# Performance work log

Hardware: AMD Instinct MI355X
Metric: run time of the kernel (lower is better)

The kernel has to match this reference:

```python
import jax, jax.numpy as jnp
import numpy as np

EPS = 1e-5

def instance_norm(x):
    # x: [B, n, C]; InstanceNorm1d normalizes over the n (length) axis per channel, no affine
    mean = jnp.mean(x, axis=1, keepdims=True)
    var = jnp.var(x, axis=1, keepdims=True)  # biased variance, matches torch
    return (x - mean) / jnp.sqrt(var + EPS)

def gat_layer(h, w, a_src, a_dst, b):
    # h: [B, n, d_in]; w: [H, d_in, d_out]; a_src/a_dst: [H, d_out, 1]; b: [d_out]
    h_ = jnp.einsum('bnd,hdk->bhnk', h, w)               # [B, H, n, d_out]
    s_src = jnp.einsum('bhnk,hk->bhn', h_, a_src[..., 0])  # [B, H, n]
    s_dst = jnp.einsum('bhnk,hk->bhn', h_, a_dst[..., 0])  # [B, H, n]
    attn = s_src[:, :, :, None] + s_dst[:, :, None, :]    # [B, H, n, n]
    attn = jax.nn.leaky_relu(attn, negative_slope=0.2)
    attn = jax.nn.softmax(attn, axis=-1)
    return jnp.einsum('bhnm,bhmk->bhnk', attn, h_) + b    # [B, H, n, d_out]

def setup_inputs() -> dict:
    key = jax.random.key(0)
    ks = jax.random.split(key, 7)
    B, N = 4, 4096
    x = jax.random.normal(ks[0], (B, N, 64), dtype=jnp.float32)
    g = 1.414
    def xavier(k, shape):
        fan_in, fan_out = shape[-2], shape[-1]
        lim = g * np.sqrt(6.0 / (fan_in + fan_out))
        return jax.random.uniform(k, shape, jnp.float32, -lim, lim)
    return {
        'x': x,
        'w0': xavier(ks[1], (4, 64, 32)),
        'a_src0': xavier(ks[2], (4, 32, 1)),
        'a_dst0': xavier(ks[3], (4, 32, 1)),
        'b0': jnp.zeros((32,), jnp.float32),
        'w1': xavier(ks[4], (1, 128, 64)),
        'a_src1': xavier(ks[5], (1, 64, 1)),
        'a_dst1': xavier(ks[6], (1, 64, 1)),
        'b1': jnp.zeros((64,), jnp.float32),
    }

def reference(x, w0, a_src0, a_dst0, b0, w1, a_src1, a_dst1, b1):
    B, N = x.shape[:2]
    # layer 0: norm -> GAT(4 heads) -> concat heads -> ELU
    h = instance_norm(x)
    h = gat_layer(h, w0, a_src0, a_dst0, b0)              # [B, 4, N, 32]
    h = jnp.transpose(h, (0, 2, 1, 3)).reshape(B, N, -1)  # [B, N, 128]
    h = jax.nn.elu(h)
    # layer 1: norm -> GAT(1 head) -> squeeze head
    h = instance_norm(h)
    h = gat_layer(h, w1, a_src1, a_dst1, b1)              # [B, 1, N, 64]
    return h[:, 0]                                        # [B, N, 64]
```

## Files before the change

kernel.cpp:

```cpp
#include <hip/hip_runtime.h>
#include <math.h>

#define N_ 4096

static constexpr size_t OFF_HP0    = 2048;
static constexpr size_t OFF_ELU    = 2048;
static constexpr size_t OFF_SS0    = 2099200;
static constexpr size_t OFF_SD0    = 2164736;
static constexpr size_t OFF_RUNS0  = 2230272;
static constexpr size_t OFF_SV0    = 2361344;
static constexpr size_t OFF_PM0    = 2426880;
static constexpr size_t OFF_EP0    = 2492416;
static constexpr size_t OFF_EN0    = 2557952;
static constexpr size_t OFF_CPP0   = 2623488;
static constexpr size_t OFF_CPN0   = 2689040;
static constexpr size_t OFF_RAWP0  = 2754592;
static constexpr size_t OFF_RAWN0  = 2885664;
static constexpr size_t OFF_BP0    = 3016736;
static constexpr size_t OFF_BN0    = 3148320;
static constexpr size_t OFF_TPP0   = 3279904;
static constexpr size_t OFF_TPN0   = 5377568;
static constexpr size_t OFF_HP1    = 3279904;
static constexpr size_t OFF_SS1    = 4328480;
static constexpr size_t OFF_SD1    = 4344864;
static constexpr size_t OFF_RUNS1  = 4361248;
static constexpr size_t OFF_SV1    = 4394016;
static constexpr size_t OFF_PM1    = 4410400;
static constexpr size_t OFF_EP1    = 4426784;
static constexpr size_t OFF_EN1    = 4443168;
static constexpr size_t OFF_CPP1   = 4459552;
static constexpr size_t OFF_CPN1   = 4475940;
static constexpr size_t OFF_RAWP1  = 4492328;
static constexpr size_t OFF_RAWN1  = 4557864;
static constexpr size_t OFF_BP1    = 4623400;
static constexpr size_t OFF_BN1    = 4689192;
static constexpr size_t OFF_TPP1   = 4754984;
static constexpr size_t OFF_TPN1   = 5803816;
static constexpr size_t OFF_S0P    = 6852648;
static constexpr size_t OFF_S1P    = 6869032;

__device__ __forceinline__ unsigned f2s(float f){
  unsigned u=__float_as_uint(f);
  return u^((u&0x80000000u)?0xFFFFFFFFu:0x80000000u);
}
__device__ __forceinline__ float s2f(unsigned s){
  unsigned u=(s&0x80000000u)?(s^0x80000000u):~s;
  return __uint_as_float(u);
}

template<int C>
__global__ void kstats(const float* __restrict__ x, float* __restrict__ statsP){
  int blk=blockIdx.x; int b=blk>>5;
  int tid=threadIdx.x;
  const int RPT=256/C;
  const int IT=128/RPT;
  int c=tid%C, rl=tid/C;
  const float* xb=x+(size_t)b*N_*C;
  float s1=0.f,s2=0.f;
  int r0=(blk&31)*128+rl;
  for(int i=0;i<IT;i++){
    float v=xb[(size_t)(r0+i*RPT)*C+c];
    s1+=v;s2+=v*v;
  }
  __shared__ float sh1[256],sh2[256];
  sh1[tid]=s1;sh2[tid]=s2;__syncthreads();
  if(tid<C){
    float a1=0.f,a2=0.f;
    for(int g=0;g<RPT;g++){a1+=sh1[g*C+tid];a2+=sh2[g*C+tid];}
    statsP[((size_t)blk*C+tid)*2+0]=a1;
    statsP[((size_t)blk*C+tid)*2+1]=a2;
  }
}

__global__ void __launch_bounds__(256) kproj0(
                       const float* __restrict__ x, const float* __restrict__ statsP,
                       const float* __restrict__ w0, const float* __restrict__ asrc,
                       const float* __restrict__ adst, float* __restrict__ hp,
                       float* __restrict__ ss, float* __restrict__ sd){
  __shared__ float4 w4[2048];
  __shared__ float4 av4[64];
  __shared__ float mean[64],rstd[64];
  __shared__ float red1[256],red2[256];
  int tid=threadIdx.x;
  const float4* wg=(const float4*)w0;
  for(int i=tid;i<2048;i+=256) w4[i]=wg[i];
  if(tid<32) av4[tid]=((const float4*)asrc)[tid];
  else if(tid<64) av4[tid]=((const float4*)adst)[tid-32];
  int gid=blockIdx.x*256+tid;
  int b=gid>>14, h=(gid>>12)&3, n=gid&4095;
  {
    int tc=tid&63, tg=tid>>6;
    float a1=0.f,a2=0.f;
    #pragma unroll 2
    for(int g=tg*8;g<tg*8+8;g++){
      a1+=statsP[((size_t)(b*32+g)*64+tc)*2+0];
      a2+=statsP[((size_t)(b*32+g)*64+tc)*2+1];
    }
    red1[tid]=a1; red2[tid]=a2;
  }
  __syncthreads();
  if(tid<64){
    float s1=red1[tid]+red1[tid+64]+red1[tid+128]+red1[tid+192];
    float s2=red2[tid]+red2[tid+64]+red2[tid+128]+red2[tid+192];
    float mu=s1*(1.0f/N_);
    float var=s2*(1.0f/N_)-mu*mu;
    mean[tid]=mu; rstd[tid]=rsqrtf(var+1e-5f);
  }
  __syncthreads();
  const float4* hr4=(const float4*)(x+((size_t)(b*N_+n))*64);
  float4 acc[8];
  #pragma unroll
  for(int q=0;q<8;q++) acc[q]=make_float4(0.f,0.f,0.f,0.f);
  #pragma unroll
  for(int ch=0;ch<4;ch++){
    float4 t[4];
    #pragma unroll
    for(int j=0;j<4;j++) t[j]=hr4[ch*4+j];
    #pragma unroll
    for(int j=0;j<4;j++){
      int d0=ch*16+j*4;
      float hv[4];
      hv[0]=(t[j].x-mean[d0+0])*rstd[d0+0];
      hv[1]=(t[j].y-mean[d0+1])*rstd[d0+1];
      hv[2]=(t[j].z-mean[d0+2])*rstd[d0+2];
      hv[3]=(t[j].w-mean[d0+3])*rstd[d0+3];
      #pragma unroll
      for(int dd=0;dd<4;dd++){
        float hvv=hv[dd];
        #pragma unroll
        for(int q=0;q<8;q++){
          float4 wv=w4[(h*64+d0+dd)*8+q];
          acc[q].x+=hvv*wv.x;acc[q].y+=hvv*wv.y;acc[q].z+=hvv*wv.z;acc[q].w+=hvv*wv.w;
        }
      }
    }
  }
  float ssv=0.f,sdv=0.f;
  #pragma unroll
  for(int q=0;q<8;q++){
    float4 a1=av4[h*8+q],a2=av4[32+h*8+q];
    ssv+=acc[q].x*a1.x+acc[q].y*a1.y+acc[q].z*a1.z+acc[q].w*a1.w;
    sdv+=acc[q].x*a2.x+acc[q].y*a2.y+acc[q].z*a2.z+acc[q].w*a2.w;
  }
  int p=b*4+h;
  float4* o4=(float4*)(hp+((size_t)p*N_+n)*32);
  #pragma unroll
  for(int q=0;q<8;q++) o4[q]=acc[q];
  ss[(size_t)p*N_+n]=ssv; sd[(size_t)p*N_+n]=sdv;
}

__global__ void __launch_bounds__(256) kproj1(
                       const float* __restrict__ x, const float* __restrict__ statsP,
                       const float* __restrict__ w1, const float* __restrict__ asrc,
                       const float* __restrict__ adst, float* __restrict__ hp,
                       float* __restrict__ ss, float* __restrict__ sd){
  __shared__ float4 w4[2048];
  __shared__ float wa[128],wd[128],mean[128],rstd[128];
  __shared__ float red1[256],red2[256];
  int tid=threadIdx.x;
  const float4* wg=(const float4*)w1;
  for(int i=tid;i<2048;i+=256) w4[i]=wg[i];
  int gid=blockIdx.x*256+tid;
  int b=gid>>14, q4=(gid>>12)&3, n=gid&4095;
  {
    int tc=tid&127, tg=tid>>7;
    float a1=0.f,a2=0.f;
    #pragma unroll 4
    for(int g=tg*16;g<tg*16+16;g++){
      a1+=statsP[((size_t)(b*32+g)*128+tc)*2+0];
      a2+=statsP[((size_t)(b*32+g)*128+tc)*2+1];
    }
    red1[tid]=a1; red2[tid]=a2;
  }
  __syncthreads();
  if(tid<128){
    float s1a=0.f,s2a=0.f;
    for(int k=0;k<64;k++){float wv=w1[tid*64+k];s1a+=wv*asrc[k];s2a+=wv*adst[k];}
    wa[tid]=s1a;wd[tid]=s2a;
    float s1=red1[tid]+red1[tid+128];
    float s2=red2[tid]+red2[tid+128];
    float mu=s1*(1.0f/N_);
    float var=s2*(1.0f/N_)-mu*mu;
    mean[tid]=mu; rstd[tid]=rsqrtf(var+1e-5f);
  }
  __syncthreads();
  const float4* hr4=(const float4*)(x+((size_t)(b*N_+n))*128);
  float4 acc[4];
  #pragma unroll
  for(int q=0;q<4;q++) acc[q]=make_float4(0.f,0.f,0.f,0.f);
  float s1=0.f,s2=0.f;
  #pragma unroll
  for(int ch=0;ch<8;ch++){
    float4 t[4];
    #pragma unroll
    for(int j=0;j<4;j++) t[j]=hr4[ch*4+j];
    #pragma unroll
    for(int j=0;j<4;j++){
      int d0=ch*16+j*4;
      float hv[4];
      hv[0]=(t[j].x-mean[d0+0])*rstd[d0+0];
      hv[1]=(t[j].y-mean[d0+1])*rstd[d0+1];
      hv[2]=(t[j].z-mean[d0+2])*rstd[d0+2];
      hv[3]=(t[j].w-mean[d0+3])*rstd[d0+3];
      #pragma unroll
      for(int dd=0;dd<4;dd++){
        float hvv=hv[dd]; int d=d0+dd;
        s1+=hvv*wa[d]; s2+=hvv*wd[d];
        #pragma unroll
        for(int q=0;q<4;q++){
          float4 wv=w4[d*16+q4*4+q];
          acc[q].x+=hvv*wv.x;acc[q].y+=hvv*wv.y;acc[q].z+=hvv*wv.z;acc[q].w+=hvv*wv.w;
        }
      }
    }
  }
  float4* o4=(float4*)(hp+((size_t)(b*N_+n))*64+q4*16);
  #pragma unroll
  for(int q=0;q<4;q++) o4[q]=acc[q];
  if(q4==0){
    ss[(size_t)b*N_+n]=s1;sd[(size_t)b*N_+n]=s2;
  }
}

__global__ void __launch_bounds__(256) ksort_runs(const float* __restrict__ sdst,
                                                  unsigned long long* __restrict__ runs){
  __shared__ unsigned long long sm[1024];
  int p=blockIdx.x>>2, run=blockIdx.x&3;
  int tid=threadIdx.x;
  const float* s=sdst+(size_t)p*N_+run*1024;
  for(int l=tid;l<1024;l+=256){
    unsigned key=f2s(s[l]);
    sm[l]=((unsigned long long)key<<32)|(unsigned)(run*1024+l);
  }
  for(unsigned k=2;k<=1024u;k<<=1)
    for(unsigned j=k>>1;j>0;j>>=1){
      __syncthreads();
      for(unsigned t=tid;t<512u;t+=256u){
        unsigned i=((t&~(j-1))<<1)|(t&(j-1));
        unsigned q=i|j;
        bool up=((i&k)==0);
        unsigned long long a=sm[i],b=sm[q];
        if((a>b)==up){sm[i]=b;sm[q]=a;}
      }
    }
  __syncthreads();
  unsigned long long* rg=runs+(size_t)p*N_+run*1024;
  for(int l=tid;l<1024;l+=256) rg[l]=sm[l];
}

__global__ void __launch_bounds__(1024) kmerge(const unsigned long long* __restrict__ runs,
    float* __restrict__ sv, unsigned* __restrict__ perm,
    float* __restrict__ eP, float* __restrict__ eN){
  __shared__ unsigned long long sm[4096];
  int p=blockIdx.x>>2, cg=blockIdx.x&3;
  int tid=threadIdx.x;
  const unsigned long long* rg=runs+(size_t)p*N_;
  for(int l=tid;l<4096;l+=1024) sm[l]=rg[l];
  __syncthreads();
  unsigned long long e=sm[cg*1024+tid];
  int rank=tid;
  #pragma unroll
  for(int o=0;o<4;o++){
    if(o==cg) continue;
    const unsigned long long* base=sm+o*1024;
    int lo=0,hi=1024;
    while(lo<hi){int mid=(lo+hi)>>1; if(base[mid]<e) lo=mid+1; else hi=mid;}
    rank+=lo;
  }
  unsigned long long mk=sm[1023];
  if(sm[2047]>mk) mk=sm[2047];
  if(sm[3071]>mk) mk=sm[3071];
  if(sm[4095]>mk) mk=sm[4095];
  float m=s2f((unsigned)(mk>>32));
  float v=s2f((unsigned)(e>>32));
  size_t o=(size_t)p*N_+rank;
  sv[o]=v;
  perm[o]=(unsigned)(e&0xffffffffu);
  eP[o]=expf(v-m);
  eN[o]=expf(0.2f*(v-m));
}

__global__ void __launch_bounds__(1024) kcounts(const float* __restrict__ eP,
    const float* __restrict__ eN, float* __restrict__ CPP, float* __restrict__ CPN){
  __shared__ float sp[1024],sn[1024];
  int p=blockIdx.x, t=threadIdx.x;
  float4 e4=((const float4*)(eP+(size_t)p*N_))[t];
  float4 n4=((const float4*)(eN+(size_t)p*N_))[t];
  float lp=e4.x+e4.y+e4.z+e4.w;
  float ln=n4.x+n4.y+n4.z+n4.w;
  sp[t]=lp; sn[t]=ln; __syncthreads();
  for(int off=1;off<1024;off<<=1){
    float vp=(t>=off)?sp[t-off]:0.f;
    float vn=(t>=off)?sn[t-off]:0.f;
    __syncthreads();
    sp[t]+=vp; sn[t]+=vn;
    __syncthreads();
  }
  float bp=sp[t]-lp, bn=sn[t]-ln;
  size_t o=(size_t)p*4097+t*4;
  float a=bp;          CPP[o+0]=a;
  a+=e4.x;             CPP[o+1]=a;
  a+=e4.y;             CPP[o+2]=a;
  a+=e4.z;             CPP[o+3]=a;
  a=bn;                CPN[o+0]=a;
  a+=n4.x;             CPN[o+1]=a;
  a+=n4.y;             CPN[o+2]=a;
  a+=n4.z;             CPN[o+3]=a;
  if(t==1023){CPP[(size_t)p*4097+4096]=sp[1023]; CPN[(size_t)p*4097+4096]=sn[1023];}
}

__global__ void __launch_bounds__(256) ktables0(const unsigned* __restrict__ perm,
    const float* __restrict__ eP, const float* __restrict__ eN,
    const float* __restrict__ hp, float* __restrict__ TPP, float* __restrict__ TPN,
    float* __restrict__ rawP, float* __restrict__ rawN){
  int gw=(blockIdx.x*256+threadIdx.x)>>6;
  int lane=threadIdx.x&63, half=lane>>5, ch=lane&31;
  int cglob=gw*2+half;
  int p=cglob>>8, c=cglob&255;
  float aP=0.f,aN=0.f;
  for(int q=0;q<16;q++){
    int r=c*16+q;
    size_t ro=(size_t)p*N_+r;
    float ep=eP[ro],en=eN[ro];
    unsigned pr=perm[ro];
    float hv=hp[((size_t)p*N_+pr)*32+ch];
    size_t to=((size_t)p*4097+r)*32+ch;
    TPP[to]=aP; TPN[to]=aN;
    aP+=ep*hv; aN+=en*hv;
  }
  size_t bo=((size_t)p*256+c)*32+ch;
  rawP[bo]=aP; rawN[bo]=aN;
}

__global__ void __launch_bounds__(256) ktables1(const unsigned* __restrict__ perm,
    const float* __restrict__ eP, const float* __restrict__ eN,
    const float* __restrict__ hp, float* __restrict__ TPP, float* __restrict__ TPN,
    float* __restrict__ rawP, float* __restrict__ rawN){
  int wid=(blockIdx.x*256+threadIdx.x)>>6;
  int lane=threadIdx.x&63;
  int p=wid>>8, c=wid&255;
  float aP=0.f,aN=0.f;
  for(int q=0;q<16;q++){
    int r=c*16+q;
    size_t ro=(size_t)p*N_+r;
    float ep=eP[ro],en=eN[ro];
    unsigned pr=perm[ro];
    float hv=hp[((size_t)p*N_+pr)*64+lane];
    size_t to=((size_t)p*4097+r)*64+lane;
    TPP[to]=aP; TPN[to]=aN;
    aP+=ep*hv; aN+=en*hv;
  }
  size_t bo=((size_t)p*256+c)*64+lane;
  rawP[bo]=aP; rawN[bo]=aN;
}

template<int D>
__global__ void __launch_bounds__(256) kscan(const float* __restrict__ rawP,
    const float* __restrict__ rawN, float* __restrict__ bP, float* __restrict__ bN,
    float* __restrict__ TPP, float* __restrict__ TPN){
  extern __shared__ float sm[];
  int p=blockIdx.x, tid=threadIdx.x;
  for(int pass=0;pass<2;pass++){
    const float* src=pass?rawN:rawP;
    float* dst=pass?bN:bP;
    float* tp=pass?TPN:TPP;
    __syncthreads();
    for(int i=tid;i<256*D;i+=256){
      sm[i]=src[(size_t)p*256*D+i];
    }
    __syncthreads();
    if(tid<D){
      float r=0.f;
      for(int c=0;c<256;c++){
        dst[((size_t)p*257+c)*D+tid]=r;
        r+=sm[c*D+tid];
      }
      dst[((size_t)p*257+256)*D+tid]=0.f;
      tp[((size_t)p*4097+4096)*D+tid]=r;
    }
  }
}

__global__ void __launch_bounds__(256) keval0(const float* __restrict__ ss,
                       const float* __restrict__ sv,
                       const float* __restrict__ bP, const float* __restrict__ bN,
                       const float* __restrict__ TPP, const float* __restrict__ TPN,
                       const float* __restrict__ CPP, const float* __restrict__ CPN,
                       const float* __restrict__ bias, float* __restrict__ out){
  int gw=(blockIdx.x*256+threadIdx.x)>>6;
  int lane=threadIdx.x&63, half=lane>>5, ch=lane&31;
  int row=gw*2+half;
  int p=row>>12, i=row&4095;
  int b=p>>2, h=p&3;
  const float* svp=sv+(size_t)p*N_;
  float ssrc=ss[(size_t)p*N_+i];
  float m=svp[4095];
  float xx=ssrc+m;
  float M=xx>0.f?xx:0.2f*xx;
  float fpos=expf(xx-M),fneg=expf(0.2f*xx-M);
  float th=-ssrc;
  float s1v=svp[ch*128+127];
  unsigned long long bal=__ballot(s1v<=th);
  int c1=half?(int)__popcll(bal>>32):(int)__popcll(bal&0xFFFFFFFFull);
  int lo;
  if(c1>=32){ lo=4096; }
  else{
    float s2v=svp[c1*128+ch*4+3];
    unsigned long long bal2=__ballot(s2v<=th);
    int c2=half?(int)__popcll(bal2>>32):(int)__popcll(bal2&0xFFFFFFFFull);
    int base=c1*128+c2*4;
    float4 qv=*((const float4*)(svp+base));
    int c3=(qv.x<=th)+(qv.y<=th)+(qv.z<=th)+(qv.w<=th);
    lo=base+c3;
  }
  int c=lo>>4;
  float relP=TPP[((size_t)p*4097+lo)*32+ch];
  float relN=TPN[((size_t)p*4097+lo)*32+ch];
  float baP=bP[((size_t)p*257+c)*32+ch];
  float baN=bN[((size_t)p*257+c)*32+ch];
  float tot=TPP[((size_t)p*4097+4096)*32+ch];
  float CPl=CPP[(size_t)p*4097+lo];
  float CNl=CPN[(size_t)p*4097+lo];
  float CT =CPP[(size_t)p*4097+4096];
  float denom=fpos*(CT-CPl)+fneg*CNl;
  float v=fpos*(tot-(baP+relP))+fneg*(baN+relN);
  float r=v/denom+bias[ch];
  r=r>0.f?r:expm1f(r);
  out[((size_t)(b*N_+i))*128+h*32+ch]=r;
}

__global__ void __launch_bounds__(256) keval1(const float* __restrict__ ss,
                       const float* __restrict__ sv,
                       const float* __restrict__ bP, const float* __restrict__ bN,
                       const float* __restrict__ TPP, const float* __restrict__ TPN,
                       const float* __restrict__ CPP, const float* __restrict__ CPN,
                       const float* __restrict__ bias, float* __restrict__ out){
  int wid=(blockIdx.x*256+threadIdx.x)>>6;
  int lane=threadIdx.x&63;
  int p=wid>>12, i=wid&4095;
  const float* svp=sv+(size_t)p*N_;
  float ssrc=ss[(size_t)p*N_+i];
  float m=svp[4095];
  float xx=ssrc+m;
  float M=xx>0.f?xx:0.2f*xx;
  float fpos=expf(xx-M),fneg=expf(0.2f*xx-M);
  float th=-ssrc;
  float s1v=svp[lane*64+63];
  int c1=(int)__popcll(__ballot(s1v<=th));
  int lo;
  if(c1>=64){ lo=4096; }
  else{
    float s2v=svp[c1*64+lane];
    lo=c1*64+(int)__popcll(__ballot(s2v<=th));
  }
  int c=lo>>4;
  float relP=TPP[((size_t)p*4097+lo)*64+lane];
  float relN=TPN[((size_t)p*4097+lo)*64+lane];
  float baP=bP[((size_t)p*257+c)*64+lane];
  float baN=bN[((size_t)p*257+c)*64+lane];
  float tot=TPP[((size_t)p*4097+4096)*64+lane];
  float CPl=CPP[(size_t)p*4097+lo];
  float CNl=CPN[(size_t)p*4097+lo];
  float CT =CPP[(size_t)p*4097+4096];
  float denom=fpos*(CT-CPl)+fneg*CNl;
  float v=fpos*(tot-(baP+relP))+fneg*(baN+relN);
  out[((size_t)p*N_+i)*64+lane]=v/denom+bias[lane];
}

extern "C" void kernel_launch(void* const* d_in, const int* in_sizes, int n_in,
                              void* d_out, int out_size, void* d_ws, size_t ws_size,
                              hipStream_t stream) {
  const float* x  =(const float*)d_in[0];
  const float* w0 =(const float*)d_in[1];
  const float* as0=(const float*)d_in[2];
  const float* ad0=(const float*)d_in[3];
  const float* b0 =(const float*)d_in[4];
  const float* w1 =(const float*)d_in[5];
  const float* as1=(const float*)d_in[6];
  const float* ad1=(const float*)d_in[7];
  const float* b1 =(const float*)d_in[8];
  float* ws=(float*)d_ws;
  float* out=(float*)d_out;

  float* s0p = ws+OFF_S0P;
  float* s1p = ws+OFF_S1P;
  float* hp0 = ws+OFF_HP0;
  float* elu = ws+OFF_ELU;
  float* ss0 = ws+OFF_SS0;  float* sd0 = ws+OFF_SD0;
  unsigned long long* runs0=(unsigned long long*)(ws+OFF_RUNS0);
  float* sv0 = ws+OFF_SV0;
  unsigned* pm0=(unsigned*)(ws+OFF_PM0);
  float* eP0 = ws+OFF_EP0;  float* eN0 = ws+OFF_EN0;
  float* cP0 = ws+OFF_CPP0; float* cN0 = ws+OFF_CPN0;
  float* rP0 = ws+OFF_RAWP0; float* rN0 = ws+OFF_RAWN0;
  float* bP0 = ws+OFF_BP0;  float* bN0 = ws+OFF_BN0;
  float* tP0 = ws+OFF_TPP0; float* tN0 = ws+OFF_TPN0;
  float* hp1 = ws+OFF_HP1;
  float* ss1 = ws+OFF_SS1;  float* sd1 = ws+OFF_SD1;
  unsigned long long* runs1=(unsigned long long*)(ws+OFF_RUNS1);
  float* sv1 = ws+OFF_SV1;
  unsigned* pm1=(unsigned*)(ws+OFF_PM1);
  float* eP1 = ws+OFF_EP1;  float* eN1 = ws+OFF_EN1;
  float* cP1 = ws+OFF_CPP1; float* cN1 = ws+OFF_CPN1;
  float* rP1 = ws+OFF_RAWP1; float* rN1 = ws+OFF_RAWN1;
  float* bP1 = ws+OFF_BP1;  float* bN1 = ws+OFF_BN1;
  float* tP1 = ws+OFF_TPP1; float* tN1 = ws+OFF_TPN1;

  kstats<64><<<128,256,0,stream>>>(x,s0p);
  kproj0<<<256,256,0,stream>>>(x,s0p,w0,as0,ad0,hp0,ss0,sd0);
  ksort_runs<<<64,256,0,stream>>>(sd0,runs0);
  kmerge<<<64,1024,0,stream>>>(runs0,sv0,pm0,eP0,eN0);
  kcounts<<<16,1024,0,stream>>>(eP0,eN0,cP0,cN0);
  ktables0<<<512,256,0,stream>>>(pm0,eP0,eN0,hp0,tP0,tN0,rP0,rN0);
  kscan<32><<<16,256,256*32*4,stream>>>(rP0,rN0,bP0,bN0,tP0,tN0);
  keval0<<<8192,256,0,stream>>>(ss0,sv0,bP0,bN0,tP0,tN0,cP0,cN0,b0,elu);
  kstats<128><<<128,256,0,stream>>>(elu,s1p);
  kproj1<<<256,256,0,stream>>>(elu,s1p,w1,as1,ad1,hp1,ss1,sd1);
  ksort_runs<<<16,256,0,stream>>>(sd1,runs1);
  kmerge<<<16,1024,0,stream>>>(runs1,sv1,pm1,eP1,eN1);
  kcounts<<<4,1024,0,stream>>>(eP1,eN1,cP1,cN1);
  ktables1<<<256,256,0,stream>>>(pm1,eP1,eN1,hp1,tP1,tN1,rP1,rN1);
  kscan<64><<<4,256,256*64*4,stream>>>(rP1,rN1,bP1,bN1,tP1,tN1);
  keval1<<<4096,256,0,stream>>>(ss1,sv1,bP1,bN1,tP1,tN1,cP1,cN1,b1,out);
}
```

Measured before the change: 231.7 us.

## Fuse prefix-count kernel into tables, parallelize block scan, drop LDS weight staging

The separate kcounts launch is folded into ktables0/ktables1 as extra leading blocks that compute the per-head exp prefix sums with 256 threads. The block-offset scan now splits positive and negative passes across blocks and parallelizes the 256-chunk serial scan over all threads using segment sums. The projection kernels stop copying the weight matrix into shared memory and read weights directly from global/cache, with blocks mapped to a single head. The aim is to remove a launch and serial scan latency, at the cost of more global weight reads.

Result: slower. 251.3 us (+8.5%).

```diff
diff --git a/kernel.cpp b/kernel.cpp
--- a/kernel.cpp
+++ b/kernel.cpp
@@ -77,17 +77,12 @@
                        const float* __restrict__ w0, const float* __restrict__ asrc,
                        const float* __restrict__ adst, float* __restrict__ hp,
                        float* __restrict__ ss, float* __restrict__ sd){
-  __shared__ float4 w4[2048];
-  __shared__ float4 av4[64];
   __shared__ float mean[64],rstd[64];
   __shared__ float red1[256],red2[256];
   int tid=threadIdx.x;
-  const float4* wg=(const float4*)w0;
-  for(int i=tid;i<2048;i+=256) w4[i]=wg[i];
-  if(tid<32) av4[tid]=((const float4*)asrc)[tid];
-  else if(tid<64) av4[tid]=((const float4*)adst)[tid-32];
-  int gid=blockIdx.x*256+tid;
-  int b=gid>>14, h=(gid>>12)&3, n=gid&4095;
+  int blk=blockIdx.x;
+  int b=blk>>6, h=(blk>>4)&3, nb=blk&15;
+  int n=nb*256+tid;
   {
     int tc=tid&63, tg=tid>>6;
     float a1=0.f,a2=0.f;
@@ -107,6 +102,9 @@
     mean[tid]=mu; rstd[tid]=rsqrtf(var+1e-5f);
   }
   __syncthreads();
+  const float4* wv4=(const float4*)(w0+(size_t)h*2048);
+  const float4* av1=(const float4*)(asrc+(size_t)h*32);
+  const float4* av2=(const float4*)(adst+(size_t)h*32);
   const float4* hr4=(const float4*)(x+((size_t)(b*N_+n))*64);
   float4 acc[8];
   #pragma unroll
@@ -129,7 +127,7 @@
         float hvv=hv[dd];
         #pragma unroll
         for(int q=0;q<8;q++){
-          float4 wv=w4[(h*64+d0+dd)*8+q];
+          float4 wv=wv4[(d0+dd)*8+q];
           acc[q].x+=hvv*wv.x;acc[q].y+=hvv*wv.y;acc[q].z+=hvv*wv.z;acc[q].w+=hvv*wv.w;
         }
       }
@@ -138,7 +136,7 @@
   float ssv=0.f,sdv=0.f;
   #pragma unroll
   for(int q=0;q<8;q++){
-    float4 a1=av4[h*8+q],a2=av4[32+h*8+q];
+    float4 a1=av1[q],a2=av2[q];
     ssv+=acc[q].x*a1.x+acc[q].y*a1.y+acc[q].z*a1.z+acc[q].w*a1.w;
     sdv+=acc[q].x*a2.x+acc[q].y*a2.y+acc[q].z*a2.z+acc[q].w*a2.w;
   }
@@ -154,14 +152,12 @@
                        const float* __restrict__ w1, const float* __restrict__ asrc,
                        const float* __restrict__ adst, float* __restrict__ hp,
                        float* __restrict__ ss, float* __restrict__ sd){
-  __shared__ float4 w4[2048];
   __shared__ float wa[128],wd[128],mean[128],rstd[128];
   __shared__ float red1[256],red2[256];
   int tid=threadIdx.x;
-  const float4* wg=(const float4*)w1;
-  for(int i=tid;i<2048;i+=256) w4[i]=wg[i];
-  int gid=blockIdx.x*256+tid;
-  int b=gid>>14, q4=(gid>>12)&3, n=gid&4095;
+  int blk=blockIdx.x;
+  int b=blk>>6, q4=(blk>>4)&3, nb=blk&15;
+  int n=nb*256+tid;
   {
     int tc=tid&127, tg=tid>>7;
     float a1=0.f,a2=0.f;
@@ -184,6 +180,7 @@
     mean[tid]=mu; rstd[tid]=rsqrtf(var+1e-5f);
   }
   __syncthreads();
+  const float4* wv4=(const float4*)w1;
   const float4* hr4=(const float4*)(x+((size_t)(b*N_+n))*128);
   float4 acc[4];
   #pragma unroll
@@ -208,7 +205,7 @@
         s1+=hvv*wa[d]; s2+=hvv*wd[d];
         #pragma unroll
         for(int q=0;q<4;q++){
-          float4 wv=w4[d*16+q4*4+q];
+          float4 wv=wv4[d*16+q4*4+q];
           acc[q].x+=hvv*wv.x;acc[q].y+=hvv*wv.y;acc[q].z+=hvv*wv.z;acc[q].w+=hvv*wv.w;
         }
       }
@@ -280,40 +277,43 @@
   eN[o]=expf(0.2f*(v-m));
 }
 
-__global__ void __launch_bounds__(1024) kcounts(const float* __restrict__ eP,
-    const float* __restrict__ eN, float* __restrict__ CPP, float* __restrict__ CPN){
-  __shared__ float sp[1024],sn[1024];
-  int p=blockIdx.x, t=threadIdx.x;
-  float4 e4=((const float4*)(eP+(size_t)p*N_))[t];
-  float4 n4=((const float4*)(eN+(size_t)p*N_))[t];
-  float lp=e4.x+e4.y+e4.z+e4.w;
-  float ln=n4.x+n4.y+n4.z+n4.w;
-  sp[t]=lp; sn[t]=ln; __syncthreads();
-  for(int off=1;off<1024;off<<=1){
-    float vp=(t>=off)?sp[t-off]:0.f;
-    float vn=(t>=off)?sn[t-off]:0.f;
-    __syncthreads();
-    sp[t]+=vp; sn[t]+=vn;
-    __syncthreads();
-  }
-  float bp=sp[t]-lp, bn=sn[t]-ln;
-  size_t o=(size_t)p*4097+t*4;
-  float a=bp;          CPP[o+0]=a;
-  a+=e4.x;             CPP[o+1]=a;
-  a+=e4.y;             CPP[o+2]=a;
-  a+=e4.z;             CPP[o+3]=a;
-  a=bn;                CPN[o+0]=a;
-  a+=n4.x;             CPN[o+1]=a;
-  a+=n4.y;             CPN[o+2]=a;
-  a+=n4.z;             CPN[o+3]=a;
-  if(t==1023){CPP[(size_t)p*4097+4096]=sp[1023]; CPN[(size_t)p*4097+4096]=sn[1023];}
+__device__ __forceinline__ void counts_block(const float* __restrict__ eP,
+    const float* __restrict__ eN, float* __restrict__ CPP, float* __restrict__ CPN,
+    int p, float* s){
+  int t=threadIdx.x;
+  for(int pass=0;pass<2;pass++){
+    const float* e=pass?eN:eP;
+    float* C=pass?CPN:CPP;
+    const float4* e4=(const float4*)(e+(size_t)p*N_);
+    float4 a0=e4[t*4+0],a1=e4[t*4+1],a2=e4[t*4+2],a3=e4[t*4+3];
+    float lp=a0.x+a0.y+a0.z+a0.w+a1.x+a1.y+a1.z+a1.w
+            +a2.x+a2.y+a2.z+a2.w+a3.x+a3.y+a3.z+a3.w;
+    if(pass) __syncthreads();
+    s[t]=lp; __syncthreads();
+    for(int off=1;off<256;off<<=1){
+      float tv=(t>=off)?s[t-off]:0.f;
+      __syncthreads();
+      s[t]+=tv;
+      __syncthreads();
+    }
+    float bp=s[t]-lp;
+    size_t o=(size_t)p*4097+(size_t)t*16;
+    C[o+ 0]=bp; bp+=a0.x; C[o+ 1]=bp; bp+=a0.y; C[o+ 2]=bp; bp+=a0.z; C[o+ 3]=bp; bp+=a0.w;
+    C[o+ 4]=bp; bp+=a1.x; C[o+ 5]=bp; bp+=a1.y; C[o+ 6]=bp; bp+=a1.z; C[o+ 7]=bp; bp+=a1.w;
+    C[o+ 8]=bp; bp+=a2.x; C[o+ 9]=bp; bp+=a2.y; C[o+10]=bp; bp+=a2.z; C[o+11]=bp; bp+=a2.w;
+    C[o+12]=bp; bp+=a3.x; C[o+13]=bp; bp+=a3.y; C[o+14]=bp; bp+=a3.z; C[o+15]=bp;
+    if(t==255) C[(size_t)p*4097+4096]=s[255];
+  }
 }
 
 __global__ void __launch_bounds__(256) ktables0(const unsigned* __restrict__ perm,
     const float* __restrict__ eP, const float* __restrict__ eN,
     const float* __restrict__ hp, float* __restrict__ TPP, float* __restrict__ TPN,
-    float* __restrict__ rawP, float* __restrict__ rawN){
-  int gw=(blockIdx.x*256+threadIdx.x)>>6;
+    float* __restrict__ rawP, float* __restrict__ rawN,
+    float* __restrict__ CPP, float* __restrict__ CPN){
+  __shared__ float s[256];
+  if(blockIdx.x<16){ counts_block(eP,eN,CPP,CPN,blockIdx.x,s); return; }
+  int gw=((blockIdx.x-16)*256+threadIdx.x)>>6;
   int lane=threadIdx.x&63, half=lane>>5, ch=lane&31;
   int cglob=gw*2+half;
   int p=cglob>>8, c=cglob&255;
@@ -335,8 +335,11 @@
 __global__ void __launch_bounds__(256) ktables1(const unsigned* __restrict__ perm,
     const float* __restrict__ eP, const float* __restrict__ eN,
     const float* __restrict__ hp, float* __restrict__ TPP, float* __restrict__ TPN,
-    float* __restrict__ rawP, float* __restrict__ rawN){
-  int wid=(blockIdx.x*256+threadIdx.x)>>6;
+    float* __restrict__ rawP, float* __restrict__ rawN,
+    float* __restrict__ CPP, float* __restrict__ CPN){
+  __shared__ float s[256];
+  if(blockIdx.x<4){ counts_block(eP,eN,CPP,CPN,blockIdx.x,s); return; }
+  int wid=((blockIdx.x-4)*256+threadIdx.x)>>6;
   int lane=threadIdx.x&63;
   int p=wid>>8, c=wid&255;
   float aP=0.f,aN=0.f;
@@ -358,26 +361,29 @@
 __global__ void __launch_bounds__(256) kscan(const float* __restrict__ rawP,
     const float* __restrict__ rawN, float* __restrict__ bP, float* __restrict__ bN,
     float* __restrict__ TPP, float* __restrict__ TPN){
-  extern __shared__ float sm[];
-  int p=blockIdx.x, tid=threadIdx.x;
-  for(int pass=0;pass<2;pass++){
-    const float* src=pass?rawN:rawP;
-    float* dst=pass?bN:bP;
-    float* tp=pass?TPN:TPP;
-    __syncthreads();
-    for(int i=tid;i<256*D;i+=256){
-      sm[i]=src[(size_t)p*256*D+i];
-    }
-    __syncthreads();
-    if(tid<D){
-      float r=0.f;
-      for(int c=0;c<256;c++){
-        dst[((size_t)p*257+c)*D+tid]=r;
-        r+=sm[c*D+tid];
-      }
-      dst[((size_t)p*257+256)*D+tid]=0.f;
-      tp[((size_t)p*4097+4096)*D+tid]=r;
-    }
+  __shared__ float ssum[256];
+  int p=blockIdx.x>>1, pass=blockIdx.x&1;
+  const float* src=pass?rawN:rawP;
+  float* dst=pass?bN:bP;
+  float* tp=pass?TPN:TPP;
+  int tid=threadIdx.x;
+  constexpr int SEG=256/D;
+  int ch=tid&(D-1), sg=tid/D;
+  const float* s0=src+(size_t)p*256*D;
+  float acc=0.f;
+  for(int c=sg*D;c<sg*D+D;c++) acc+=s0[c*D+ch];
+  ssum[tid]=acc; __syncthreads();
+  float base=0.f, tot=0.f;
+  #pragma unroll
+  for(int g=0;g<SEG;g++){float v=ssum[g*D+ch]; tot+=v; if(g<sg) base+=v;}
+  float r=base;
+  for(int c=sg*D;c<sg*D+D;c++){
+    dst[((size_t)p*257+c)*D+ch]=r;
+    r+=s0[c*D+ch];
+  }
+  if(sg==0){
+    dst[((size_t)p*257+256)*D+ch]=0.f;
+    tp[((size_t)p*4097+4096)*D+ch]=tot;
   }
 }
 
@@ -510,16 +516,14 @@
   kproj0<<<256,256,0,stream>>>(x,s0p,w0,as0,ad0,hp0,ss0,sd0);
   ksort_runs<<<64,256,0,stream>>>(sd0,runs0);
   kmerge<<<64,1024,0,stream>>>(runs0,sv0,pm0,eP0,eN0);
-  kcounts<<<16,1024,0,stream>>>(eP0,eN0,cP0,cN0);
-  ktables0<<<512,256,0,stream>>>(pm0,eP0,eN0,hp0,tP0,tN0,rP0,rN0);
-  kscan<32><<<16,256,256*32*4,stream>>>(rP0,rN0,bP0,bN0,tP0,tN0);
+  ktables0<<<528,256,0,stream>>>(pm0,eP0,eN0,hp0,tP0,tN0,rP0,rN0,cP0,cN0);
+  kscan<32><<<32,256,0,stream>>>(rP0,rN0,bP0,bN0,tP0,tN0);
   keval0<<<8192,256,0,stream>>>(ss0,sv0,bP0,bN0,tP0,tN0,cP0,cN0,b0,elu);
   kstats<128><<<128,256,0,stream>>>(elu,s1p);
   kproj1<<<256,256,0,stream>>>(elu,s1p,w1,as1,ad1,hp1,ss1,sd1);
   ksort_runs<<<16,256,0,stream>>>(sd1,runs1);
   kmerge<<<16,1024,0,stream>>>(runs1,sv1,pm1,eP1,eN1);
-  kcounts<<<4,1024,0,stream>>>(eP1,eN1,cP1,cN1);
-  ktables1<<<256,256,0,stream>>>(pm1,eP1,eN1,hp1,tP1,tN1,rP1,rN1);
-  kscan<64><<<4,256,256*64*4,stream>>>(rP1,rN1,bP1,bN1,tP1,tN1);
+  ktables1<<<260,256,0,stream>>>(pm1,eP1,eN1,hp1,tP1,tN1,rP1,rN1,cP1,cN1);
+  kscan<64><<<8,256,0,stream>>>(rP1,rN1,bP1,bN1,tP1,tN1);
   keval1<<<4096,256,0,stream>>>(ss1,sv1,bP1,bN1,tP1,tN1,cP1,cN1,b1,out);
 }
```
